# Optimization experiments

Measured on AMD Instinct MI355X. Metric: run time of the kernel, lower is better.

## Reference

```python
import jax, jax.numpy as jnp
import numpy as np

MODEL_DIM = 768
EMB_DIM = 768
NUM_HEADS = 12
HEAD_DIM = MODEL_DIM // NUM_HEADS  # 64
B, S = 4, 1024
LN_EPS = 1e-12


def setup_inputs() -> dict:
    key = jax.random.key(0)
    ks = jax.random.split(key, 12)
    s_in = 1.0 / np.sqrt(EMB_DIM)
    s_dm = 1.0 / np.sqrt(MODEL_DIM)
    return {
        "x": jax.random.normal(ks[0], (B, S, EMB_DIM), dtype=jnp.float32),
        # stacked per-head projection weights, [H, E, Dh] (in, out layout)
        "Wq": jax.random.normal(ks[1], (NUM_HEADS, EMB_DIM, HEAD_DIM), dtype=jnp.float32) * s_in,
        "bq": jax.random.normal(ks[2], (NUM_HEADS, HEAD_DIM), dtype=jnp.float32) * 0.02,
        "Wk": jax.random.normal(ks[3], (NUM_HEADS, EMB_DIM, HEAD_DIM), dtype=jnp.float32) * s_in,
        "bk": jax.random.normal(ks[4], (NUM_HEADS, HEAD_DIM), dtype=jnp.float32) * 0.02,
        "Wv": jax.random.normal(ks[5], (NUM_HEADS, EMB_DIM, HEAD_DIM), dtype=jnp.float32) * s_in,
        "bv": jax.random.normal(ks[6], (NUM_HEADS, HEAD_DIM), dtype=jnp.float32) * 0.02,
        # output dense [Dm, Dm] (in, out) + bias
        "Wd": jax.random.normal(ks[7], (MODEL_DIM, MODEL_DIM), dtype=jnp.float32) * s_dm,
        "bd": jax.random.normal(ks[8], (MODEL_DIM,), dtype=jnp.float32) * 0.02,
        # LayerNorm affine params
        "gamma": jnp.ones((MODEL_DIM,), dtype=jnp.float32),
        "beta": jnp.zeros((MODEL_DIM,), dtype=jnp.float32),
    }


def reference(x, Wq, bq, Wk, bk, Wv, bv, Wd, bd, gamma, beta):
    # Batched per-head projections: [B,S,E] x [H,E,Dh] -> [B,H,S,Dh]
    Q = jnp.einsum("bse,hed->bhsd", x, Wq) + bq[None, :, None, :]
    K = jnp.einsum("bse,hed->bhsd", x, Wk) + bk[None, :, None, :]
    V = jnp.einsum("bse,hed->bhsd", x, Wv) + bv[None, :, None, :]

    scale = 1.0 / jnp.sqrt(jnp.asarray(HEAD_DIM, dtype=Q.dtype))
    scores = jnp.einsum("bhsd,bhtd->bhst", Q, K) * scale  # [B,H,S,S]
    weights = jax.nn.softmax(scores, axis=-1)
    ctx = jnp.einsum("bhst,bhtd->bhsd", weights, V)  # [B,H,S,Dh]

    # concat per-head outputs along last dim (head order): [B,S,H*Dh]
    outputs = jnp.transpose(ctx, (0, 2, 1, 3)).reshape(B, S, NUM_HEADS * HEAD_DIM)
    # concat per-head attention weights along last dim: [B,S,H*S]
    weights_cat = jnp.transpose(weights, (0, 2, 1, 3)).reshape(B, S, NUM_HEADS * S)

    # BertSelfOutput: dense -> LayerNorm (dropout = identity in eval)
    y = jnp.einsum("bsi,io->bso", outputs, Wd) + bd
    mu = jnp.mean(y, axis=-1, keepdims=True)
    var = jnp.mean(jnp.square(y - mu), axis=-1, keepdims=True)
    y = (y - mu) * jax.lax.rsqrt(var + LN_EPS) * gamma + beta
    return weights_cat, y
```

## Files before the change

kernel.cpp:

```cpp
#include <hip/hip_runtime.h>

typedef __bf16 bf16x8 __attribute__((ext_vector_type(8)));
typedef float  f32x4  __attribute__((ext_vector_type(4)));
typedef unsigned short u16x8 __attribute__((ext_vector_type(8)));
typedef unsigned short u16x4 __attribute__((ext_vector_type(4)));

__device__ __forceinline__ unsigned short f2bf(float f) {
  union { float f; unsigned u; } v; v.f = f;
  unsigned r = v.u + 0x7fffu + ((v.u >> 16) & 1u);
  return (unsigned short)(r >> 16);
}

__device__ __forceinline__ float bf2f(unsigned short b) {
  union { unsigned u; float f; } v; v.u = (unsigned)b << 16;
  return v.f;
}

__device__ __forceinline__ void gload16(const unsigned short* g, unsigned short* l) {
  __builtin_amdgcn_global_load_lds(
      (const __attribute__((address_space(1))) unsigned int*)g,
      (__attribute__((address_space(3))) unsigned int*)l,
      16, 0, 0);
}

#define WOFF 50331648

__global__ void convert_x(const float* __restrict__ in, unsigned short* __restrict__ outb) {
  int i = (blockIdx.x * 256 + threadIdx.x) * 8;
  f32x4 v0 = *(const f32x4*)&in[i];
  f32x4 v1 = *(const f32x4*)&in[i + 4];
  u16x8 o;
  for (int j = 0; j < 4; j++) { o[j] = f2bf(v0[j]); o[j + 4] = f2bf(v1[j]); }
  *(u16x8*)&outb[i] = o;
}

__global__ void transpose_qkv(const float* __restrict__ Wq, const float* __restrict__ Wk,
                              const float* __restrict__ Wv, unsigned short* __restrict__ outb) {
  __shared__ float t[32][33];
  int z = blockIdx.z;
  int m = z / 12;
  const float* in = (m == 0 ? Wq : m == 1 ? Wk : Wv) + (long)(z % 12) * 49152;
  unsigned short* ob = outb + (long)z * 49152;
  int c  = blockIdx.x * 32 + threadIdx.x;
  int r0 = blockIdx.y * 32;
  for (int i = threadIdx.y; i < 32; i += 8)
    t[i][threadIdx.x] = in[(long)(r0 + i) * 64 + c];
  __syncthreads();
  int c0 = blockIdx.x * 32;
  for (int i = threadIdx.y; i < 32; i += 8)
    ob[(long)(c0 + i) * 768 + r0 + threadIdx.x] = f2bf(t[threadIdx.x][i]);
}

__global__ void transpose_f32_bf16(const float* __restrict__ in, unsigned short* __restrict__ outb,
                                   int R, int C) {
  __shared__ float t[32][33];
  int c  = blockIdx.x * 32 + threadIdx.x;
  int r0 = blockIdx.y * 32;
  for (int i = threadIdx.y; i < 32; i += 8)
    t[i][threadIdx.x] = in[(long)(r0 + i) * C + c];
  __syncthreads();
  int c0 = blockIdx.x * 32;
  for (int i = threadIdx.y; i < 32; i += 8)
    outb[(long)(c0 + i) * R + r0 + threadIdx.x] = f2bf(t[threadIdx.x][i]);
}

__global__ __launch_bounds__(256) void qkv_gemm(
    const unsigned short* __restrict__ xb, const unsigned short* __restrict__ wb,
    const float* __restrict__ bq, const float* __restrict__ bk, const float* __restrict__ bv,
    unsigned short* __restrict__ Qb, unsigned short* __restrict__ Kb, unsigned short* __restrict__ Vt)
{
  __shared__ unsigned short As[4096];
  __shared__ unsigned short Bs[4096];
  const int tid = threadIdx.x;
  const int bn = blockIdx.x * 128, bm = blockIdx.y * 128;
  const int w = tid >> 6, l = tid & 63;
  const int wr = w >> 1, wc = w & 1;
  const int lr = l & 15, lg = l >> 4;

  f32x4 acc[4][4];
  for (int i = 0; i < 4; i++) for (int j = 0; j < 4; j++) acc[i][j] = {0.f, 0.f, 0.f, 0.f};

  const unsigned short* ga = xb + (long)(bm + (tid >> 2)) * 768 + (tid & 3) * 8;
  const unsigned short* gb = wb + (long)(bn + (tid >> 2)) * 768 + (tid & 3) * 8;
  unsigned short* lA = As + (w << 9);
  unsigned short* lB = Bs + (w << 9);

  for (int k0 = 0; k0 < 768; k0 += 32) {
    gload16(ga + k0,            lA);
    gload16(ga + k0 + 64 * 768, lA + 2048);
    gload16(gb + k0,            lB);
    gload16(gb + k0 + 64 * 768, lB + 2048);
    __syncthreads();
    bf16x8 af[4], bfv[4];
    for (int i = 0; i < 4; i++) af[i]  = *(const bf16x8*)&As[(wr * 64 + i * 16 + lr) * 32 + lg * 8];
    for (int j = 0; j < 4; j++) bfv[j] = *(const bf16x8*)&Bs[(wc * 64 + j * 16 + lr) * 32 + lg * 8];
    for (int i = 0; i < 4; i++)
      for (int j = 0; j < 4; j++)
        acc[i][j] = __builtin_amdgcn_mfma_f32_16x16x32_bf16(af[i], bfv[j], acc[i][j], 0, 0, 0);
    __syncthreads();
  }

  for (int i = 0; i < 4; i++) for (int j = 0; j < 4; j++) {
    int col = bn + wc * 64 + j * 16 + lr;
    int m = col / 768, rc = col % 768;
    int h = rc >> 6, d = rc & 63;
    const float* bias = (m == 0) ? bq : (m == 1) ? bk : bv;
    float bb = bias[rc];
    for (int r = 0; r < 4; r++) {
      int row = bm + wr * 64 + i * 16 + lg * 4 + r;
      int b = row >> 10, s = row & 1023;
      float v = acc[i][j][r] + bb;
      if (m == 0)      Qb[((b * 12 + h) << 16) + (s << 6) + d] = f2bf(v * 0.125f);
      else if (m == 1) Kb[((b * 12 + h) << 16) + (s << 6) + d] = f2bf(v);
      else             Vt[((b * 12 + h) << 16) + (d << 10) + s] = f2bf(v);
    }
  }
}

__global__ __launch_bounds__(512) void attn_kernel(
    const unsigned short* __restrict__ Qb, const unsigned short* __restrict__ Kb,
    const unsigned short* __restrict__ Vt,
    float* __restrict__ wout, unsigned short* __restrict__ ctx)
{
  extern __shared__ char smem[];
  unsigned short* E  = (unsigned short*)smem;
  unsigned short* Qs = (unsigned short*)(smem + 66048);
  float* sred = (float*)(smem + 70656);
  float* sfin = (float*)(smem + 71680);

  const int q0 = blockIdx.x * 32;
  const int bh = blockIdx.y;
  const int b = bh / 12, h = bh % 12;
  const int tid = threadIdx.x;
  const int w = tid >> 6, l = tid & 63, lr = l & 15, lg = l >> 4;
  const unsigned short* Qg = Qb + (bh << 16);
  const unsigned short* Kg = Kb + (bh << 16);
  const unsigned short* Vg = Vt + (bh << 16);

  if (tid < 256) {
    int row = tid >> 3, c = (tid & 7) * 8;
    *(u16x8*)&Qs[row * 72 + c] = *(const u16x8*)&Qg[(q0 + row) * 64 + c];
  }
  __syncthreads();

  bf16x8 qa[2][2];
  for (int ri = 0; ri < 2; ri++) {
    qa[ri][0] = *(const bf16x8*)&Qs[(ri * 16 + lr) * 72 + lg * 8];
    qa[ri][1] = *(const bf16x8*)&Qs[(ri * 16 + lr) * 72 + 32 + lg * 8];
  }
  f32x4 sc[2][8];
#pragma unroll
  for (int cf = 0; cf < 8; cf++) {
    int colb = w * 128 + cf * 16;
    bf16x8 kb0 = *(const bf16x8*)&Kg[(colb + lr) * 64 + lg * 8];
    bf16x8 kb1 = *(const bf16x8*)&Kg[(colb + lr) * 64 + 32 + lg * 8];
#pragma unroll
    for (int ri = 0; ri < 2; ri++) {
      f32x4 a = {0.f, 0.f, 0.f, 0.f};
      a = __builtin_amdgcn_mfma_f32_16x16x32_bf16(qa[ri][0], kb0, a, 0, 0, 0);
      a = __builtin_amdgcn_mfma_f32_16x16x32_bf16(qa[ri][1], kb1, a, 0, 0, 0);
      sc[ri][cf] = a;
    }
  }

  float sm[2][4] = {{0.f, 0.f, 0.f, 0.f}, {0.f, 0.f, 0.f, 0.f}};
#pragma unroll
  for (int cf = 0; cf < 8; cf++)
#pragma unroll
    for (int ri = 0; ri < 2; ri++)
#pragma unroll
      for (int r = 0; r < 4; r++) {
        float e = __expf(sc[ri][cf][r]);
        sm[ri][r] += e;
        E[(ri * 16 + lg * 4 + r) * 1032 + w * 128 + cf * 16 + lr] = f2bf(e);
      }
#pragma unroll
  for (int ri = 0; ri < 2; ri++)
#pragma unroll
    for (int r = 0; r < 4; r++) {
      float s = sm[ri][r];
      for (int o = 8; o >= 1; o >>= 1) s += __shfl_xor(s, o, 16);
      if (lr == 0) sred[w * 32 + ri * 16 + lg * 4 + r] = s;
    }
  __syncthreads();
  if (tid < 32) {
    float s = 0.f;
    for (int ww = 0; ww < 8; ww++) s += sred[ww * 32 + tid];
    sfin[tid] = 1.f / s;
  }
  __syncthreads();

  {
    float* wbase = wout + (long)(b * 1024 + q0) * 12288 + h * 1024;
#pragma unroll
    for (int it = 0; it < 16; it++) {
      int vidx = it * 512 + tid;
      int row = vidx >> 8, c4 = (vidx & 255) * 4;
      float rs = sfin[row];
      u16x4 ev = *(const u16x4*)&E[row * 1032 + c4];
      f32x4 o;
      for (int t = 0; t < 4; t++) o[t] = bf2f(ev[t]) * rs;
      *(f32x4*)&wbase[(long)row * 12288 + c4] = o;
    }
  }

  {
    int ri = w >> 2, cf = w & 3;
    f32x4 acc = {0.f, 0.f, 0.f, 0.f};
#pragma unroll
    for (int ks = 0; ks < 32; ks++) {
      int kk = ks * 32;
      bf16x8 pa = *(const bf16x8*)&E[(ri * 16 + lr) * 1032 + kk + lg * 8];
      bf16x8 vb = *(const bf16x8*)&Vg[(cf * 16 + lr) * 1024 + kk + lg * 8];
      acc = __builtin_amdgcn_mfma_f32_16x16x32_bf16(pa, vb, acc, 0, 0, 0);
    }
    for (int r = 0; r < 4; r++) {
      int row = ri * 16 + lg * 4 + r;
      Qs[row * 72 + cf * 16 + lr] = f2bf(acc[r] * sfin[row]);
    }
  }
  __syncthreads();
  if (tid < 256) {
    int row = tid >> 3, c = (tid & 7) * 8;
    *(u16x8*)&ctx[(long)(b * 1024 + q0 + row) * 768 + h * 64 + c] = *(const u16x8*)&Qs[row * 72 + c];
  }
}

__global__ __launch_bounds__(256) void dense_gemm(
    const unsigned short* __restrict__ ctx, const unsigned short* __restrict__ wdb,
    float* __restrict__ y)
{
  __shared__ unsigned short As[4096];
  __shared__ unsigned short Bs[4096];
  const int tid = threadIdx.x;
  const int bn = blockIdx.x * 128, bm = blockIdx.y * 128;
  const int w = tid >> 6, l = tid & 63;
  const int wr = w >> 1, wc = w & 1;
  const int lr = l & 15, lg = l >> 4;

  f32x4 acc[4][4];
  for (int i = 0; i < 4; i++) for (int j = 0; j < 4; j++) acc[i][j] = {0.f, 0.f, 0.f, 0.f};

  const unsigned short* ga = ctx + (long)(bm + (tid >> 2)) * 768 + (tid & 3) * 8;
  const unsigned short* gb = wdb + (long)(bn + (tid >> 2)) * 768 + (tid & 3) * 8;
  unsigned short* lA = As + (w << 9);
  unsigned short* lB = Bs + (w << 9);

  for (int k0 = 0; k0 < 768; k0 += 32) {
    gload16(ga + k0,            lA);
    gload16(ga + k0 + 64 * 768, lA + 2048);
    gload16(gb + k0,            lB);
    gload16(gb + k0 + 64 * 768, lB + 2048);
    __syncthreads();
    bf16x8 af[4], bfv[4];
    for (int i = 0; i < 4; i++) af[i]  = *(const bf16x8*)&As[(wr * 64 + i * 16 + lr) * 32 + lg * 8];
    for (int j = 0; j < 4; j++) bfv[j] = *(const bf16x8*)&Bs[(wc * 64 + j * 16 + lr) * 32 + lg * 8];
    for (int i = 0; i < 4; i++)
      for (int j = 0; j < 4; j++)
        acc[i][j] = __builtin_amdgcn_mfma_f32_16x16x32_bf16(af[i], bfv[j], acc[i][j], 0, 0, 0);
    __syncthreads();
  }

  for (int i = 0; i < 4; i++) for (int j = 0; j < 4; j++) {
    int col = bn + wc * 64 + j * 16 + lr;
    for (int r = 0; r < 4; r++) {
      int row = bm + wr * 64 + i * 16 + lg * 4 + r;
      y[(long)row * 768 + col] = acc[i][j][r];
    }
  }
}

__global__ __launch_bounds__(256) void ln_kernel(
    const float* __restrict__ y, const float* __restrict__ bd,
    const float* __restrict__ gamma, const float* __restrict__ beta,
    float* __restrict__ out)
{
  int w = threadIdx.x >> 6, l = threadIdx.x & 63;
  long row = blockIdx.x * 4 + w;
  const float* yr = y + row * 768;
  f32x4 v[3];
  float s = 0.f, ss = 0.f;
  for (int j = 0; j < 3; j++) {
    int c = j * 256 + l * 4;
    f32x4 t = *(const f32x4*)&yr[c];
    f32x4 bb = *(const f32x4*)&bd[c];
    for (int q = 0; q < 4; q++) { t[q] += bb[q]; s += t[q]; ss += t[q] * t[q]; }
    v[j] = t;
  }
  for (int o = 32; o >= 1; o >>= 1) { s += __shfl_xor(s, o); ss += __shfl_xor(ss, o); }
  float mu = s * (1.f / 768.f);
  float var = ss * (1.f / 768.f) - mu * mu;
  float rs = rsqrtf(var + 1e-12f);
  float* orow = out + row * 768;
  for (int j = 0; j < 3; j++) {
    int c = j * 256 + l * 4;
    f32x4 g = *(const f32x4*)&gamma[c];
    f32x4 be = *(const f32x4*)&beta[c];
    f32x4 o;
    for (int q = 0; q < 4; q++) o[q] = (v[j][q] - mu) * rs * g[q] + be[q];
    *(f32x4*)&orow[c] = o;
  }
}

extern "C" void kernel_launch(void* const* d_in, const int* in_sizes, int n_in,
                              void* d_out, int out_size, void* d_ws, size_t ws_size,
                              hipStream_t stream) {
  const float* x     = (const float*)d_in[0];
  const float* Wq    = (const float*)d_in[1];
  const float* bq    = (const float*)d_in[2];
  const float* Wk    = (const float*)d_in[3];
  const float* bk    = (const float*)d_in[4];
  const float* Wv    = (const float*)d_in[5];
  const float* bv    = (const float*)d_in[6];
  const float* Wd    = (const float*)d_in[7];
  const float* bd    = (const float*)d_in[8];
  const float* gamma = (const float*)d_in[9];
  const float* beta  = (const float*)d_in[10];
  float* out = (float*)d_out;

  char* ws = (char*)d_ws;
  unsigned short* xb  = (unsigned short*)(ws);
  unsigned short* wb  = (unsigned short*)(ws + 6291456);
  unsigned short* wdb = (unsigned short*)(ws + 9830400);
  unsigned short* Qb  = (unsigned short*)(ws + 11010048);
  unsigned short* Kb  = (unsigned short*)(ws + 17301504);
  unsigned short* Vt  = (unsigned short*)(ws + 23592960);
  unsigned short* ctx = (unsigned short*)(ws + 29884416);
  float*          yws = (float*)(ws + 11010048);

  convert_x<<<1536, 256, 0, stream>>>(x, xb);
  dim3 tb(32, 8);
  transpose_qkv<<<dim3(2, 24, 36), tb, 0, stream>>>(Wq, Wk, Wv, wb);
  transpose_f32_bf16<<<dim3(24, 24, 1), tb, 0, stream>>>(Wd, wdb, 768, 768);
  qkv_gemm<<<dim3(18, 32), 256, 0, stream>>>(xb, wb, bq, bk, bv, Qb, Kb, Vt);
  attn_kernel<<<dim3(32, 48), 512, 71808, stream>>>(Qb, Kb, Vt, out, ctx);
  dense_gemm<<<dim3(6, 32), 256, 0, stream>>>(ctx, wdb, yws);
  ln_kernel<<<1024, 256, 0, stream>>>(yws, bd, gamma, beta, out + WOFF);
}
```

Before: 163.2 us.

## Merge prep kernels, double-buffer GEMMs, shrink dense tile, nontemporal output stores

Merges the three conversion and transpose kernels into one launch and double-buffers the LDS tiles in both GEMMs, so the next K-slice loads while MFMAs run on the current one. The dense GEMM tile shrinks to 64 rows to double its grid, and the dense bias moves into the GEMM epilogue. The large attention-weights output and the LayerNorm output now use nontemporal stores to avoid polluting cache. The costs are more LDS per block and smaller per-block reuse in the dense GEMM.

```diff
diff --git a/kernel.cpp b/kernel.cpp
--- a/kernel.cpp
+++ b/kernel.cpp
@@ -23,45 +23,52 @@
       16, 0, 0);
 }
 
+__device__ __forceinline__ void nt_store4(float* p, f32x4 v) {
+  __builtin_nontemporal_store(v, (f32x4*)p);
+}
+
 #define WOFF 50331648
 
-__global__ void convert_x(const float* __restrict__ in, unsigned short* __restrict__ outb) {
-  int i = (blockIdx.x * 256 + threadIdx.x) * 8;
-  f32x4 v0 = *(const f32x4*)&in[i];
-  f32x4 v1 = *(const f32x4*)&in[i + 4];
-  u16x8 o;
-  for (int j = 0; j < 4; j++) { o[j] = f2bf(v0[j]); o[j + 4] = f2bf(v1[j]); }
-  *(u16x8*)&outb[i] = o;
-}
-
-__global__ void transpose_qkv(const float* __restrict__ Wq, const float* __restrict__ Wk,
-                              const float* __restrict__ Wv, unsigned short* __restrict__ outb) {
+__global__ __launch_bounds__(256) void prep(
+    const float* __restrict__ x, const float* __restrict__ Wq, const float* __restrict__ Wk,
+    const float* __restrict__ Wv, const float* __restrict__ Wd,
+    unsigned short* __restrict__ xb, unsigned short* __restrict__ wb, unsigned short* __restrict__ wdb)
+{
   __shared__ float t[32][33];
-  int z = blockIdx.z;
-  int m = z / 12;
-  const float* in = (m == 0 ? Wq : m == 1 ? Wk : Wv) + (long)(z % 12) * 49152;
-  unsigned short* ob = outb + (long)z * 49152;
-  int c  = blockIdx.x * 32 + threadIdx.x;
-  int r0 = blockIdx.y * 32;
-  for (int i = threadIdx.y; i < 32; i += 8)
-    t[i][threadIdx.x] = in[(long)(r0 + i) * 64 + c];
-  __syncthreads();
-  int c0 = blockIdx.x * 32;
-  for (int i = threadIdx.y; i < 32; i += 8)
-    ob[(long)(c0 + i) * 768 + r0 + threadIdx.x] = f2bf(t[threadIdx.x][i]);
-}
-
-__global__ void transpose_f32_bf16(const float* __restrict__ in, unsigned short* __restrict__ outb,
-                                   int R, int C) {
-  __shared__ float t[32][33];
-  int c  = blockIdx.x * 32 + threadIdx.x;
-  int r0 = blockIdx.y * 32;
-  for (int i = threadIdx.y; i < 32; i += 8)
-    t[i][threadIdx.x] = in[(long)(r0 + i) * C + c];
-  __syncthreads();
-  int c0 = blockIdx.x * 32;
-  for (int i = threadIdx.y; i < 32; i += 8)
-    outb[(long)(c0 + i) * R + r0 + threadIdx.x] = f2bf(t[threadIdx.x][i]);
+  const int bid = blockIdx.x, tid = threadIdx.x;
+  if (bid < 1536) {
+    int i = (bid * 256 + tid) * 8;
+    f32x4 v0 = *(const f32x4*)&x[i];
+    f32x4 v1 = *(const f32x4*)&x[i + 4];
+    u16x8 o;
+    for (int j = 0; j < 4; j++) { o[j] = f2bf(v0[j]); o[j + 4] = f2bf(v1[j]); }
+    *(u16x8*)&xb[i] = o;
+    return;
+  }
+  const int tx = tid & 31, ty = tid >> 5;
+  if (bid < 3264) {
+    int q = bid - 1536;
+    int bx = q & 1; q >>= 1;
+    int by = q % 24, z = q / 24;
+    int m = z / 12;
+    const float* in = (m == 0 ? Wq : m == 1 ? Wk : Wv) + (long)(z % 12) * 49152;
+    unsigned short* ob = wb + (long)z * 49152;
+    int c = bx * 32 + tx, r0 = by * 32;
+    for (int i = ty; i < 32; i += 8) t[i][tx] = in[(long)(r0 + i) * 64 + c];
+    __syncthreads();
+    int c0 = bx * 32;
+    for (int i = ty; i < 32; i += 8) ob[(long)(c0 + i) * 768 + r0 + tx] = f2bf(t[tx][i]);
+    return;
+  }
+  {
+    int q = bid - 3264;
+    int bx = q % 24, by = q / 24;
+    int c = bx * 32 + tx, r0 = by * 32;
+    for (int i = ty; i < 32; i += 8) t[i][tx] = Wd[(long)(r0 + i) * 768 + c];
+    __syncthreads();
+    int c0 = bx * 32;
+    for (int i = ty; i < 32; i += 8) wdb[(long)(c0 + i) * 768 + r0 + tx] = f2bf(t[tx][i]);
+  }
 }
 
 __global__ __launch_bounds__(256) void qkv_gemm(
@@ -69,8 +76,8 @@
     const float* __restrict__ bq, const float* __restrict__ bk, const float* __restrict__ bv,
     unsigned short* __restrict__ Qb, unsigned short* __restrict__ Kb, unsigned short* __restrict__ Vt)
 {
-  __shared__ unsigned short As[4096];
-  __shared__ unsigned short Bs[4096];
+  __shared__ unsigned short As[2][4096];
+  __shared__ unsigned short Bs[2][4096];
   const int tid = threadIdx.x;
   const int bn = blockIdx.x * 128, bm = blockIdx.y * 128;
   const int w = tid >> 6, l = tid & 63;
@@ -82,22 +89,31 @@
 
   const unsigned short* ga = xb + (long)(bm + (tid >> 2)) * 768 + (tid & 3) * 8;
   const unsigned short* gb = wb + (long)(bn + (tid >> 2)) * 768 + (tid & 3) * 8;
-  unsigned short* lA = As + (w << 9);
-  unsigned short* lB = Bs + (w << 9);
-
-  for (int k0 = 0; k0 < 768; k0 += 32) {
-    gload16(ga + k0,            lA);
-    gload16(ga + k0 + 64 * 768, lA + 2048);
-    gload16(gb + k0,            lB);
-    gload16(gb + k0 + 64 * 768, lB + 2048);
-    __syncthreads();
+  const int lofs = w << 9;
+
+  gload16(ga,            &As[0][lofs]);
+  gload16(ga + 64 * 768, &As[0][lofs + 2048]);
+  gload16(gb,            &Bs[0][lofs]);
+  gload16(gb + 64 * 768, &Bs[0][lofs + 2048]);
+  __syncthreads();
+
+  int cur = 0;
+  for (int t = 0; t < 24; t++) {
+    if (t < 23) {
+      int k0 = (t + 1) * 32;
+      gload16(ga + k0,            &As[cur ^ 1][lofs]);
+      gload16(ga + k0 + 64 * 768, &As[cur ^ 1][lofs + 2048]);
+      gload16(gb + k0,            &Bs[cur ^ 1][lofs]);
+      gload16(gb + k0 + 64 * 768, &Bs[cur ^ 1][lofs + 2048]);
+    }
     bf16x8 af[4], bfv[4];
-    for (int i = 0; i < 4; i++) af[i]  = *(const bf16x8*)&As[(wr * 64 + i * 16 + lr) * 32 + lg * 8];
-    for (int j = 0; j < 4; j++) bfv[j] = *(const bf16x8*)&Bs[(wc * 64 + j * 16 + lr) * 32 + lg * 8];
+    for (int i = 0; i < 4; i++) af[i]  = *(const bf16x8*)&As[cur][(wr * 64 + i * 16 + lr) * 32 + lg * 8];
+    for (int j = 0; j < 4; j++) bfv[j] = *(const bf16x8*)&Bs[cur][(wc * 64 + j * 16 + lr) * 32 + lg * 8];
     for (int i = 0; i < 4; i++)
       for (int j = 0; j < 4; j++)
         acc[i][j] = __builtin_amdgcn_mfma_f32_16x16x32_bf16(af[i], bfv[j], acc[i][j], 0, 0, 0);
     __syncthreads();
+    cur ^= 1;
   }
 
   for (int i = 0; i < 4; i++) for (int j = 0; j < 4; j++) {
@@ -200,7 +216,7 @@
       u16x4 ev = *(const u16x4*)&E[row * 1032 + c4];
       f32x4 o;
       for (int t = 0; t < 4; t++) o[t] = bf2f(ev[t]) * rs;
-      *(f32x4*)&wbase[(long)row * 12288 + c4] = o;
+      nt_store4(&wbase[(long)row * 12288 + c4], o);
     }
   }
 
@@ -228,50 +244,58 @@
 
 __global__ __launch_bounds__(256) void dense_gemm(
     const unsigned short* __restrict__ ctx, const unsigned short* __restrict__ wdb,
-    float* __restrict__ y)
-{
-  __shared__ unsigned short As[4096];
-  __shared__ unsigned short Bs[4096];
+    const float* __restrict__ bd, float* __restrict__ y)
+{
+  __shared__ unsigned short As[2][2048];
+  __shared__ unsigned short Bs[2][4096];
   const int tid = threadIdx.x;
-  const int bn = blockIdx.x * 128, bm = blockIdx.y * 128;
+  const int bn = blockIdx.x * 128, bm = blockIdx.y * 64;
   const int w = tid >> 6, l = tid & 63;
   const int wr = w >> 1, wc = w & 1;
   const int lr = l & 15, lg = l >> 4;
 
-  f32x4 acc[4][4];
-  for (int i = 0; i < 4; i++) for (int j = 0; j < 4; j++) acc[i][j] = {0.f, 0.f, 0.f, 0.f};
+  f32x4 acc[2][4];
+  for (int i = 0; i < 2; i++) for (int j = 0; j < 4; j++) acc[i][j] = {0.f, 0.f, 0.f, 0.f};
 
   const unsigned short* ga = ctx + (long)(bm + (tid >> 2)) * 768 + (tid & 3) * 8;
   const unsigned short* gb = wdb + (long)(bn + (tid >> 2)) * 768 + (tid & 3) * 8;
-  unsigned short* lA = As + (w << 9);
-  unsigned short* lB = Bs + (w << 9);
-
-  for (int k0 = 0; k0 < 768; k0 += 32) {
-    gload16(ga + k0,            lA);
-    gload16(ga + k0 + 64 * 768, lA + 2048);
-    gload16(gb + k0,            lB);
-    gload16(gb + k0 + 64 * 768, lB + 2048);
-    __syncthreads();
-    bf16x8 af[4], bfv[4];
-    for (int i = 0; i < 4; i++) af[i]  = *(const bf16x8*)&As[(wr * 64 + i * 16 + lr) * 32 + lg * 8];
-    for (int j = 0; j < 4; j++) bfv[j] = *(const bf16x8*)&Bs[(wc * 64 + j * 16 + lr) * 32 + lg * 8];
-    for (int i = 0; i < 4; i++)
+  const int lofs = w << 9;
+
+  gload16(ga,            &As[0][lofs]);
+  gload16(gb,            &Bs[0][lofs]);
+  gload16(gb + 64 * 768, &Bs[0][lofs + 2048]);
+  __syncthreads();
+
+  int cur = 0;
+  for (int t = 0; t < 24; t++) {
+    if (t < 23) {
+      int k0 = (t + 1) * 32;
+      gload16(ga + k0,            &As[cur ^ 1][lofs]);
+      gload16(gb + k0,            &Bs[cur ^ 1][lofs]);
+      gload16(gb + k0 + 64 * 768, &Bs[cur ^ 1][lofs + 2048]);
+    }
+    bf16x8 af[2], bfv[4];
+    for (int i = 0; i < 2; i++) af[i]  = *(const bf16x8*)&As[cur][(wr * 32 + i * 16 + lr) * 32 + lg * 8];
+    for (int j = 0; j < 4; j++) bfv[j] = *(const bf16x8*)&Bs[cur][(wc * 64 + j * 16 + lr) * 32 + lg * 8];
+    for (int i = 0; i < 2; i++)
       for (int j = 0; j < 4; j++)
         acc[i][j] = __builtin_amdgcn_mfma_f32_16x16x32_bf16(af[i], bfv[j], acc[i][j], 0, 0, 0);
     __syncthreads();
-  }
-
-  for (int i = 0; i < 4; i++) for (int j = 0; j < 4; j++) {
+    cur ^= 1;
+  }
+
+  for (int i = 0; i < 2; i++) for (int j = 0; j < 4; j++) {
     int col = bn + wc * 64 + j * 16 + lr;
+    float bb = bd[col];
     for (int r = 0; r < 4; r++) {
-      int row = bm + wr * 64 + i * 16 + lg * 4 + r;
-      y[(long)row * 768 + col] = acc[i][j][r];
+      int row = bm + wr * 32 + i * 16 + lg * 4 + r;
+      y[(long)row * 768 + col] = acc[i][j][r] + bb;
     }
   }
 }
 
 __global__ __launch_bounds__(256) void ln_kernel(
-    const float* __restrict__ y, const float* __restrict__ bd,
+    const float* __restrict__ y,
     const float* __restrict__ gamma, const float* __restrict__ beta,
     float* __restrict__ out)
 {
@@ -283,8 +307,7 @@
   for (int j = 0; j < 3; j++) {
     int c = j * 256 + l * 4;
     f32x4 t = *(const f32x4*)&yr[c];
-    f32x4 bb = *(const f32x4*)&bd[c];
-    for (int q = 0; q < 4; q++) { t[q] += bb[q]; s += t[q]; ss += t[q] * t[q]; }
+    for (int q = 0; q < 4; q++) { s += t[q]; ss += t[q] * t[q]; }
     v[j] = t;
   }
   for (int o = 32; o >= 1; o >>= 1) { s += __shfl_xor(s, o); ss += __shfl_xor(ss, o); }
@@ -298,7 +321,7 @@
     f32x4 be = *(const f32x4*)&beta[c];
     f32x4 o;
     for (int q = 0; q < 4; q++) o[q] = (v[j][q] - mu) * rs * g[q] + be[q];
-    *(f32x4*)&orow[c] = o;
+    nt_store4(&orow[c], o);
   }
 }
 
@@ -328,12 +351,9 @@
   unsigned short* ctx = (unsigned short*)(ws + 29884416);
   float*          yws = (float*)(ws + 11010048);
 
-  convert_x<<<1536, 256, 0, stream>>>(x, xb);
-  dim3 tb(32, 8);
-  transpose_qkv<<<dim3(2, 24, 36), tb, 0, stream>>>(Wq, Wk, Wv, wb);
-  transpose_f32_bf16<<<dim3(24, 24, 1), tb, 0, stream>>>(Wd, wdb, 768, 768);
+  prep<<<3840, 256, 0, stream>>>(x, Wq, Wk, Wv, Wd, xb, wb, wdb);
   qkv_gemm<<<dim3(18, 32), 256, 0, stream>>>(xb, wb, bq, bk, bv, Qb, Kb, Vt);
   attn_kernel<<<dim3(32, 48), 512, 71808, stream>>>(Qb, Kb, Vt, out, ctx);
-  dense_gemm<<<dim3(6, 32), 256, 0, stream>>>(ctx, wdb, yws);
-  ln_kernel<<<1024, 256, 0, stream>>>(yws, bd, gamma, beta, out + WOFF);
-}
+  dense_gemm<<<dim3(6, 64), 256, 0, stream>>>(ctx, wdb, bd, yws);
+  ln_kernel<<<1024, 256, 0, stream>>>(yws, gamma, beta, out + WOFF);
+}
```

Measured after the change: 155.5 us. 4.7% less time.
